# Kernel tuning notes

Measured on AMD Instinct MI355X. Metric: run time of the kernel, lower is better.

Reference implementation:

```python
import jax, jax.numpy as jnp
import numpy as np

D_MODEL = 1024
NUM_HEADS = 16
HEAD_DIM = D_MODEL // NUM_HEADS


def setup_inputs() -> dict:
    key = jax.random.key(0)
    ks = jax.random.split(key, 9)
    B, S, D = 2, 2048, D_MODEL
    s = 1.0 / np.sqrt(D)
    return {
        "x": jax.random.normal(ks[0], (B, S, D), dtype=jnp.float32),
        "Wq": jax.random.normal(ks[1], (D, D), dtype=jnp.float32) * s,
        "bq": jnp.zeros((D,), dtype=jnp.float32),
        "Wk": jax.random.normal(ks[2], (D, D), dtype=jnp.float32) * s,
        "bk": jnp.zeros((D,), dtype=jnp.float32),
        "Wv": jax.random.normal(ks[3], (D, D), dtype=jnp.float32) * s,
        "bv": jnp.zeros((D,), dtype=jnp.float32),
        "Wo": jax.random.normal(ks[4], (D, D), dtype=jnp.float32) * s,
        "bo": jnp.zeros((D,), dtype=jnp.float32),
    }


def reference(x, Wq, bq, Wk, bk, Wv, bv, Wo, bo):
    B, S, D = x.shape
    H, Hd = NUM_HEADS, HEAD_DIM
    # Linear projections (torch Linear: x @ W^T + b)
    q = (x @ Wq.T + bq).reshape(B, S, H, Hd).transpose(0, 2, 1, 3)  # [B,H,S,Hd]
    k = (x @ Wk.T + bk).reshape(B, S, H, Hd).transpose(0, 2, 1, 3)
    v = (x @ Wv.T + bv).reshape(B, S, H, Hd).transpose(0, 2, 1, 3)
    scale = 1.0 / jnp.sqrt(jnp.asarray(Hd, dtype=x.dtype))
    scores = jnp.einsum("bhqd,bhkd->bhqk", q, k) * scale  # [B,H,S,S]
    causal = jnp.triu(jnp.ones((S, S), dtype=bool), k=1)  # True above diagonal
    scores = jnp.where(causal[None, None], -jnp.inf, scores)
    attn = jax.nn.softmax(scores, axis=-1)
    out = jnp.einsum("bhqk,bhkd->bhqd", attn, v)  # [B,H,S,Hd]
    out = out.transpose(0, 2, 1, 3).reshape(B, S, D)
    return out @ Wo.T + bo
```

## Files before the change

kernel.cpp:

```cpp
#include <hip/hip_runtime.h>

typedef _Float16 f16x8 __attribute__((ext_vector_type(8)));
typedef _Float16 f16x4 __attribute__((ext_vector_type(4)));
typedef float f32x4 __attribute__((ext_vector_type(4)));

#define MFMA32(a, b, c) __builtin_amdgcn_mfma_f32_16x16x32_f16(a, b, c, 0, 0, 0)
#define MFMA16(a, b, c) __builtin_amdgcn_mfma_f32_16x16x16f16(a, b, c, 0, 0, 0)

__global__ __launch_bounds__(256) void convert_all(
    const float* __restrict__ x,
    const float* __restrict__ w0, const float* __restrict__ w1,
    const float* __restrict__ w2, const float* __restrict__ w3,
    _Float16* __restrict__ xb,
    _Float16* __restrict__ o0, _Float16* __restrict__ o1,
    _Float16* __restrict__ o2, _Float16* __restrict__ o3) {
  int chunk = blockIdx.x * 256 + threadIdx.x;
  const float* in;
  _Float16* out;
  int i;
  if (chunk < 1048576) {
    in = x; out = xb; i = chunk * 4;
  } else {
    int t = chunk - 1048576;
    int z = t >> 18;
    i = (t & 262143) * 4;
    in = (z == 0) ? w0 : (z == 1) ? w1 : (z == 2) ? w2 : w3;
    out = (z == 0) ? o0 : (z == 1) ? o1 : (z == 2) ? o2 : o3;
  }
  float4 v = *(const float4*)(in + i);
  f16x4 h;
  h.x = (_Float16)v.x; h.y = (_Float16)v.y; h.z = (_Float16)v.z; h.w = (_Float16)v.w;
  *(f16x4*)(out + i) = h;
}

__device__ __forceinline__ void gld_lds16(_Float16* l, const _Float16* g) {
  __builtin_amdgcn_global_load_lds(
      (const __attribute__((address_space(1))) unsigned int*)g,
      (__attribute__((address_space(3))) unsigned int*)l, 16, 0, 0);
}

__device__ __forceinline__ void stage64(_Float16* lds, const _Float16* g,
                                        int wid, int lane) {
#pragma unroll
  for (int j = 0; j < 2; ++j) {
    int blk = wid * 2 + j;
    int row = blk * 8 + (lane >> 3);
    int col = (lane & 7) * 8;
    gld_lds16(lds + blk * 512, g + (size_t)row * 1024 + col);
  }
}

__device__ __forceinline__ void stage128(_Float16* lds, const _Float16* g,
                                         int wid, int lane) {
#pragma unroll
  for (int j = 0; j < 4; ++j) {
    int blk = wid * 4 + j;
    int row = blk * 8 + (lane >> 3);
    int col = (lane & 7) * 8;
    gld_lds16(lds + blk * 512, g + (size_t)row * 1024 + col);
  }
}

__device__ __forceinline__ void gemm_core64(const _Float16* __restrict__ A,
                                            const _Float16* __restrict__ W,
                                            _Float16* As, _Float16* Bs,
                                            f32x4 acc[4][2], int m0, int n0, int tid) {
  int lane = tid & 63, wid = tid >> 6;
  int lr = lane & 15, lg = lane >> 4;
  int wn = wid * 32;
  for (int k0 = 0; k0 < 1024; k0 += 64) {
    __syncthreads();
    stage64(As, A + (size_t)m0 * 1024 + k0, wid, lane);
    stage128(Bs, W + (size_t)n0 * 1024 + k0, wid, lane);
    __syncthreads();
#pragma unroll
    for (int ks = 0; ks < 2; ++ks) {
      f16x8 af[4], bfv[2];
#pragma unroll
      for (int mf = 0; mf < 4; ++mf)
        af[mf] = *(const f16x8*)(As + (mf * 16 + lr) * 64 + ks * 32 + lg * 8);
#pragma unroll
      for (int nf = 0; nf < 2; ++nf)
        bfv[nf] = *(const f16x8*)(Bs + (wn + nf * 16 + lr) * 64 + ks * 32 + lg * 8);
#pragma unroll
      for (int mf = 0; mf < 4; ++mf)
#pragma unroll
        for (int nf = 0; nf < 2; ++nf)
          acc[mf][nf] = MFMA32(af[mf], bfv[nf], acc[mf][nf]);
    }
  }
}

#define TRP 72

__global__ __launch_bounds__(256) void proj_gemm(
    const _Float16* __restrict__ xb,
    const _Float16* __restrict__ wq, const _Float16* __restrict__ wk,
    const _Float16* __restrict__ wv,
    const float* __restrict__ bq, const float* __restrict__ bk,
    const float* __restrict__ bv,
    _Float16* __restrict__ qo, _Float16* __restrict__ ko, _Float16* __restrict__ vo) {
  __shared__ __align__(16) _Float16 smem[12288];
  _Float16* As = smem;
  _Float16* Bs = smem + 4096;
  int z = blockIdx.z;
  const _Float16* W = (z == 0) ? wq : ((z == 1) ? wk : wv);
  const float* bias = (z == 0) ? bq : ((z == 1) ? bk : bv);
  int tid = threadIdx.x;
  int m0 = blockIdx.x * 64, n0 = blockIdx.y * 128;
  f32x4 acc[4][2] = {};
  gemm_core64(xb, W, As, Bs, acc, m0, n0, tid);

  int lane = tid & 63, wid = tid >> 6;
  int lr = lane & 15, lg = lane >> 4;
  int wn = wid * 32;

  if (z == 2) {
    _Float16* Tr = smem;
    int b = m0 >> 11, s0 = m0 & 2047;
    __syncthreads();
#pragma unroll
    for (int nf = 0; nf < 2; ++nf) {
      int c = wn + nf * 16 + lr;
      float bb = bias[n0 + c];
#pragma unroll
      for (int mf = 0; mf < 4; ++mf)
#pragma unroll
        for (int i = 0; i < 4; ++i)
          Tr[c * TRP + mf * 16 + lg * 4 + i] = (_Float16)(acc[mf][nf][i] + bb);
    }
    __syncthreads();
#pragma unroll
    for (int j = 0; j < 4; ++j) {
      int cid = tid + 256 * j;
      int c = cid >> 3, seg = cid & 7;
      int cg = n0 + c, h = cg >> 6, hd = cg & 63;
      f16x8 v = *(const f16x8*)(Tr + c * TRP + seg * 8);
      *(f16x8*)(vo + ((size_t)(b * 16 + h) * 64 + hd) * 2048 + s0 + seg * 8) = v;
    }
  } else {
    _Float16* o = (z == 0) ? qo : ko;
#pragma unroll
    for (int nf = 0; nf < 2; ++nf) {
      int col = n0 + wn + nf * 16 + lr;
      float bb = bias[col];
      int h = col >> 6, hd = col & 63;
#pragma unroll
      for (int mf = 0; mf < 4; ++mf)
#pragma unroll
        for (int i = 0; i < 4; ++i) {
          int row = m0 + mf * 16 + lg * 4 + i;
          int b = row >> 11, s = row & 2047;
          o[((size_t)(b * 16 + h) * 2048 + s) * 64 + hd] = (_Float16)(acc[mf][nf][i] + bb);
        }
    }
  }
}

__global__ __launch_bounds__(256) void out_gemm(
    const _Float16* __restrict__ attn, const _Float16* __restrict__ wo,
    const float* __restrict__ bo, float* __restrict__ out) {
  __shared__ __align__(16) _Float16 smem[12288];
  _Float16* As = smem;
  _Float16* Bs = smem + 4096;
  int tid = threadIdx.x;
  int m0 = blockIdx.x * 64, n0 = blockIdx.y * 128;
  f32x4 acc[4][2] = {};
  gemm_core64(attn, wo, As, Bs, acc, m0, n0, tid);

  int lane = tid & 63, wid = tid >> 6;
  int lr = lane & 15, lg = lane >> 4;
  int wn = wid * 32;
#pragma unroll
  for (int nf = 0; nf < 2; ++nf) {
    int col = n0 + wn + nf * 16 + lr;
    float bb = bo[col];
#pragma unroll
    for (int mf = 0; mf < 4; ++mf)
#pragma unroll
      for (int i = 0; i < 4; ++i) {
        int row = m0 + mf * 16 + lg * 4 + i;
        out[(size_t)row * 1024 + col] = acc[mf][nf][i] + bb;
      }
  }
}

#define LDP 72

template <bool MASK>
__device__ __forceinline__ void attn_tile32(const _Float16* Ks, const _Float16* Vs,
                                            const f16x8 qb[2][2], int kv0, int qwb,
                                            int lr, int lg,
                                            float m[2], float l[2], f32x4 ot[2][4]) {
  const float L2E = 1.44269504f;
  const float NINF = -__builtin_inff();
  f16x8 kf0[4], kf1[4];
#pragma unroll
  for (int nf = 0; nf < 4; ++nf) {
    kf0[nf] = *(const f16x8*)(Ks + (nf * 16 + lr) * LDP + lg * 8);
    kf1[nf] = *(const f16x8*)(Ks + (nf * 16 + lr) * LDP + 32 + lg * 8);
  }
  f32x4 sc[2][4];
  __builtin_amdgcn_s_setprio(1);
#pragma unroll
  for (int h = 0; h < 2; ++h)
#pragma unroll
    for (int nf = 0; nf < 4; ++nf) {
      f32x4 z = {0.f, 0.f, 0.f, 0.f};
      z = MFMA32(kf0[nf], qb[h][0], z);
      z = MFMA32(kf1[nf], qb[h][1], z);
      sc[h][nf] = z;
    }
  __builtin_amdgcn_s_setprio(0);
  if (MASK) {
#pragma unroll
    for (int h = 0; h < 2; ++h) {
      int qg = qwb + h * 16 + lr;
#pragma unroll
      for (int nf = 0; nf < 4; ++nf)
#pragma unroll
        for (int i = 0; i < 4; ++i) {
          int kg = kv0 + nf * 16 + lg * 4 + i;
          sc[h][nf][i] = (kg <= qg) ? sc[h][nf][i] : NINF;
        }
    }
  }
  f16x4 pf[2][4];
#pragma unroll
  for (int h = 0; h < 2; ++h) {
    f32x4 mx4 = sc[h][0];
#pragma unroll
    for (int nf = 1; nf < 4; ++nf)
#pragma unroll
      for (int i = 0; i < 4; ++i) mx4[i] = fmaxf(mx4[i], sc[h][nf][i]);
    float tm = fmaxf(fmaxf(mx4[0], mx4[1]), fmaxf(mx4[2], mx4[3]));
    tm = fmaxf(tm, __shfl_xor(tm, 16));
    tm = fmaxf(tm, __shfl_xor(tm, 32));
    float mn = fmaxf(m[h], tm);
    float alpha = __builtin_amdgcn_exp2f((m[h] - mn) * L2E);
    m[h] = mn;
    float mnL = mn * L2E;
    float ps = 0.f;
#pragma unroll
    for (int nf = 0; nf < 4; ++nf)
#pragma unroll
      for (int i = 0; i < 4; ++i) {
        float p = __builtin_amdgcn_exp2f(sc[h][nf][i] * L2E - mnL);
        ps += p;
        pf[h][nf][i] = (_Float16)p;
      }
    ps += __shfl_xor(ps, 16);
    ps += __shfl_xor(ps, 32);
    l[h] = l[h] * alpha + ps;
#pragma unroll
    for (int dt = 0; dt < 4; ++dt)
#pragma unroll
      for (int i = 0; i < 4; ++i) ot[h][dt][i] *= alpha;
  }
  __builtin_amdgcn_s_setprio(1);
#pragma unroll
  for (int nf = 0; nf < 4; ++nf)
#pragma unroll
    for (int dt = 0; dt < 4; ++dt) {
      f16x4 vf = *(const f16x4*)(Vs + (dt * 16 + lr) * LDP + nf * 16 + lg * 4);
      ot[0][dt] = MFMA16(vf, pf[0][nf], ot[0][dt]);
      ot[1][dt] = MFMA16(vf, pf[1][nf], ot[1][dt]);
    }
  __builtin_amdgcn_s_setprio(0);
}

__global__ __launch_bounds__(256) void attn_kernel(
    const _Float16* __restrict__ Q, const _Float16* __restrict__ K,
    const _Float16* __restrict__ VT, _Float16* __restrict__ O) {
  __shared__ __align__(16) _Float16 Ks[2][64 * LDP];
  __shared__ __align__(16) _Float16 Vs[2][64 * LDP];
  int tid = threadIdx.x, lane = tid & 63, wid = tid >> 6;
  int qt = blockIdx.z ? (15 - (int)blockIdx.x) : (int)blockIdx.x;
  int hh = blockIdx.y, b = blockIdx.z;
  size_t hoff = (size_t)(b * 16 + hh) * 2048 * 64;
  const _Float16* Qh = Q + hoff;
  const _Float16* Kh = K + hoff;
  const _Float16* VTh = VT + hoff;
  int qwb = qt * 128 + wid * 32;
  int lr = lane & 15, lg = lane >> 4;

  f16x8 qb[2][2];
#pragma unroll
  for (int h = 0; h < 2; ++h) {
    const _Float16* qp = Qh + (size_t)(qwb + h * 16 + lr) * 64;
    qb[h][0] = *(const f16x8*)(qp + lg * 8);
    qb[h][1] = *(const f16x8*)(qp + 32 + lg * 8);
#pragma unroll
    for (int j = 0; j < 8; ++j) {
      qb[h][0][j] *= (_Float16)0.125f;
      qb[h][1][j] *= (_Float16)0.125f;
    }
  }

  float m[2] = {-__builtin_inff(), -__builtin_inff()};
  float l[2] = {0.f, 0.f};
  f32x4 ot[2][4] = {};

  int r0 = tid >> 3, c0 = (tid & 7) * 8;
  int r1 = r0 + 32;
  int4 rk0 = *(const int4*)(Kh + (size_t)r0 * 64 + c0);
  int4 rk1 = *(const int4*)(Kh + (size_t)r1 * 64 + c0);
  int4 rv0 = *(const int4*)(VTh + (size_t)r0 * 2048 + c0);
  int4 rv1 = *(const int4*)(VTh + (size_t)r1 * 2048 + c0);
  *(int4*)(&Ks[0][0] + r0 * LDP + c0) = rk0;
  *(int4*)(&Ks[0][0] + r1 * LDP + c0) = rk1;
  *(int4*)(&Vs[0][0] + r0 * LDP + c0) = rv0;
  *(int4*)(&Vs[0][0] + r1 * LDP + c0) = rv1;
  __syncthreads();

  int aw = qwb >> 6;
  int ntiles = 2 * qt + 2;
  for (int t = 0; t < ntiles; ++t) {
    int cur = t & 1;
    if (t + 1 < ntiles) {
      int nkv = (t + 1) * 64;
      rk0 = *(const int4*)(Kh + (size_t)(nkv + r0) * 64 + c0);
      rk1 = *(const int4*)(Kh + (size_t)(nkv + r1) * 64 + c0);
      rv0 = *(const int4*)(VTh + (size_t)r0 * 2048 + nkv + c0);
      rv1 = *(const int4*)(VTh + (size_t)r1 * 2048 + nkv + c0);
    }
    if (t < aw)
      attn_tile32<false>(&Ks[cur][0], &Vs[cur][0], qb, t * 64, qwb, lr, lg, m, l, ot);
    else if (t == aw)
      attn_tile32<true>(&Ks[cur][0], &Vs[cur][0], qb, t * 64, qwb, lr, lg, m, l, ot);
    if (t + 1 < ntiles) {
      *(int4*)(&Ks[cur ^ 1][0] + r0 * LDP + c0) = rk0;
      *(int4*)(&Ks[cur ^ 1][0] + r1 * LDP + c0) = rk1;
      *(int4*)(&Vs[cur ^ 1][0] + r0 * LDP + c0) = rv0;
      *(int4*)(&Vs[cur ^ 1][0] + r1 * LDP + c0) = rv1;
    }
    __syncthreads();
  }

#pragma unroll
  for (int h = 0; h < 2; ++h) {
    float inv = 1.f / l[h];
    _Float16* Oh = O + ((size_t)b * 2048 + qwb + h * 16 + lr) * 1024 + hh * 64;
#pragma unroll
    for (int dt = 0; dt < 4; ++dt) {
      f16x4 o;
#pragma unroll
      for (int i = 0; i < 4; ++i) o[i] = (_Float16)(ot[h][dt][i] * inv);
      *(f16x4*)(Oh + dt * 16 + lg * 4) = o;
    }
  }
}

extern "C" void kernel_launch(void* const* d_in, const int* in_sizes, int n_in,
                              void* d_out, int out_size, void* d_ws, size_t ws_size,
                              hipStream_t stream) {
  const float* x  = (const float*)d_in[0];
  const float* Wq = (const float*)d_in[1];
  const float* bq = (const float*)d_in[2];
  const float* Wk = (const float*)d_in[3];
  const float* bk = (const float*)d_in[4];
  const float* Wv = (const float*)d_in[5];
  const float* bv = (const float*)d_in[6];
  const float* Wo = (const float*)d_in[7];
  const float* bo = (const float*)d_in[8];
  float* out = (float*)d_out;

  _Float16* ws  = (_Float16*)d_ws;
  _Float16* xb  = ws;
  _Float16* wqb = ws + 4194304;
  _Float16* wkb = ws + 5242880;
  _Float16* wvb = ws + 6291456;
  _Float16* wob = ws + 7340032;
  _Float16* qw  = ws + 8388608;
  _Float16* kw  = ws + 12582912;
  _Float16* vtw = ws + 16777216;
  _Float16* aw  = ws + 20971520;

  convert_all<<<8192, 256, 0, stream>>>(x, Wq, Wk, Wv, Wo,
                                        xb, wqb, wkb, wvb, wob);

  proj_gemm<<<dim3(64, 8, 3), 256, 0, stream>>>(xb, wqb, wkb, wvb, bq, bk, bv,
                                                qw, kw, vtw);
  attn_kernel<<<dim3(16, 16, 2), 256, 0, stream>>>(qw, kw, vtw, aw);
  out_gemm<<<dim3(64, 8), 256, 0, stream>>>(aw, wob, bo, out);
}
```

Measured before the change: 127.6 us.

## Split causal attention KV range across two blocks and merge with combine kernel

Each query tile's causal KV range is split into two halves, each handled by its own block. The grid grows from 512 to 1024 blocks, and the causal work is balanced between the two halves. Each half writes unnormalized fp16 partial outputs plus per-row (max, sum) statistics into reused workspace buffers. A new combine kernel rescales and merges the two partials into the final attention output. The aim is more parallelism and better CU fill, at the cost of extra partial-output memory traffic, an extra launch, and fp16 storage of unnormalized accumulators.

```diff
diff --git a/kernel.cpp b/kernel.cpp
--- a/kernel.cpp
+++ b/kernel.cpp
@@ -271,12 +271,15 @@
 
 __global__ __launch_bounds__(256) void attn_kernel(
     const _Float16* __restrict__ Q, const _Float16* __restrict__ K,
-    const _Float16* __restrict__ VT, _Float16* __restrict__ O) {
+    const _Float16* __restrict__ VT,
+    _Float16* __restrict__ PO0, _Float16* __restrict__ PO1,
+    float2* __restrict__ ML) {
   __shared__ __align__(16) _Float16 Ks[2][64 * LDP];
   __shared__ __align__(16) _Float16 Vs[2][64 * LDP];
   int tid = threadIdx.x, lane = tid & 63, wid = tid >> 6;
-  int qt = blockIdx.z ? (15 - (int)blockIdx.x) : (int)blockIdx.x;
-  int hh = blockIdx.y, b = blockIdx.z;
+  int b = blockIdx.z >> 1, half = blockIdx.z & 1;
+  int qt = b ? (15 - (int)blockIdx.x) : (int)blockIdx.x;
+  int hh = blockIdx.y;
   size_t hoff = (size_t)(b * 16 + hh) * 2048 * 64;
   const _Float16* Qh = Q + hoff;
   const _Float16* Kh = K + hoff;
@@ -284,6 +287,9 @@
   int qwb = qt * 128 + wid * 32;
   int lr = lane & 15, lg = lane >> 4;
 
+  int start = half ? (qt + 1) : 0;
+  int end = half ? (2 * qt + 2) : (qt + 1);
+
   f16x8 qb[2][2];
 #pragma unroll
   for (int h = 0; h < 2; ++h) {
@@ -303,21 +309,24 @@
 
   int r0 = tid >> 3, c0 = (tid & 7) * 8;
   int r1 = r0 + 32;
-  int4 rk0 = *(const int4*)(Kh + (size_t)r0 * 64 + c0);
-  int4 rk1 = *(const int4*)(Kh + (size_t)r1 * 64 + c0);
-  int4 rv0 = *(const int4*)(VTh + (size_t)r0 * 2048 + c0);
-  int4 rv1 = *(const int4*)(VTh + (size_t)r1 * 2048 + c0);
-  *(int4*)(&Ks[0][0] + r0 * LDP + c0) = rk0;
-  *(int4*)(&Ks[0][0] + r1 * LDP + c0) = rk1;
-  *(int4*)(&Vs[0][0] + r0 * LDP + c0) = rv0;
-  *(int4*)(&Vs[0][0] + r1 * LDP + c0) = rv1;
+  {
+    int kv = start * 64;
+    int4 k0 = *(const int4*)(Kh + (size_t)(kv + r0) * 64 + c0);
+    int4 k1 = *(const int4*)(Kh + (size_t)(kv + r1) * 64 + c0);
+    int4 v0 = *(const int4*)(VTh + (size_t)r0 * 2048 + kv + c0);
+    int4 v1 = *(const int4*)(VTh + (size_t)r1 * 2048 + kv + c0);
+    *(int4*)(&Ks[0][0] + r0 * LDP + c0) = k0;
+    *(int4*)(&Ks[0][0] + r1 * LDP + c0) = k1;
+    *(int4*)(&Vs[0][0] + r0 * LDP + c0) = v0;
+    *(int4*)(&Vs[0][0] + r1 * LDP + c0) = v1;
+  }
   __syncthreads();
 
   int aw = qwb >> 6;
-  int ntiles = 2 * qt + 2;
-  for (int t = 0; t < ntiles; ++t) {
-    int cur = t & 1;
-    if (t + 1 < ntiles) {
+  int4 rk0, rk1, rv0, rv1;
+  for (int t = start; t < end; ++t) {
+    int cur = (t - start) & 1;
+    if (t + 1 < end) {
       int nkv = (t + 1) * 64;
       rk0 = *(const int4*)(Kh + (size_t)(nkv + r0) * 64 + c0);
       rk1 = *(const int4*)(Kh + (size_t)(nkv + r1) * 64 + c0);
@@ -328,7 +337,7 @@
       attn_tile32<false>(&Ks[cur][0], &Vs[cur][0], qb, t * 64, qwb, lr, lg, m, l, ot);
     else if (t == aw)
       attn_tile32<true>(&Ks[cur][0], &Vs[cur][0], qb, t * 64, qwb, lr, lg, m, l, ot);
-    if (t + 1 < ntiles) {
+    if (t + 1 < end) {
       *(int4*)(&Ks[cur ^ 1][0] + r0 * LDP + c0) = rk0;
       *(int4*)(&Ks[cur ^ 1][0] + r1 * LDP + c0) = rk1;
       *(int4*)(&Vs[cur ^ 1][0] + r0 * LDP + c0) = rv0;
@@ -337,18 +346,45 @@
     __syncthreads();
   }
 
+  _Float16* PO = half ? PO1 : PO0;
 #pragma unroll
   for (int h = 0; h < 2; ++h) {
-    float inv = 1.f / l[h];
-    _Float16* Oh = O + ((size_t)b * 2048 + qwb + h * 16 + lr) * 1024 + hh * 64;
+    int q = qwb + h * 16 + lr;
+    if (lg == 0)
+      ML[(((size_t)(half * 2 + b) * 2048 + q) << 4) + hh] = float2{m[h], l[h]};
+    _Float16* Oh = PO + ((size_t)b * 2048 + q) * 1024 + hh * 64;
 #pragma unroll
     for (int dt = 0; dt < 4; ++dt) {
       f16x4 o;
 #pragma unroll
-      for (int i = 0; i < 4; ++i) o[i] = (_Float16)(ot[h][dt][i] * inv);
+      for (int i = 0; i < 4; ++i) o[i] = (_Float16)ot[h][dt][i];
       *(f16x4*)(Oh + dt * 16 + lg * 4) = o;
     }
   }
+}
+
+__global__ __launch_bounds__(256) void attn_combine(
+    const _Float16* __restrict__ PO0, const _Float16* __restrict__ PO1,
+    const float2* __restrict__ ML, _Float16* __restrict__ Oout) {
+  const float L2E = 1.44269504f;
+  int g = blockIdx.x * 256 + threadIdx.x;
+  int row = g >> 3, chunk = g & 7;
+  float2 a = ML[row];
+  float2 c = ML[row + 65536];
+  float ms = fmaxf(a.x, c.x);
+  float f0 = __builtin_amdgcn_exp2f((a.x - ms) * L2E);
+  float f1 = __builtin_amdgcn_exp2f((c.x - ms) * L2E);
+  float inv = 1.f / (f0 * a.y + f1 * c.y);
+  f0 *= inv; f1 *= inv;
+  int b = row >> 15, q = (row >> 4) & 2047, h = row & 15;
+  size_t off = ((size_t)(b * 2048 + q) * 1024) + h * 64 + chunk * 8;
+  f16x8 o0 = *(const f16x8*)(PO0 + off);
+  f16x8 o1 = *(const f16x8*)(PO1 + off);
+  f16x8 r;
+#pragma unroll
+  for (int j = 0; j < 8; ++j)
+    r[j] = (_Float16)(f0 * (float)o0[j] + f1 * (float)o1[j]);
+  *(f16x8*)(Oout + off) = r;
 }
 
 extern "C" void kernel_launch(void* const* d_in, const int* in_sizes, int n_in,
@@ -376,11 +412,15 @@
   _Float16* vtw = ws + 16777216;
   _Float16* aw  = ws + 20971520;
 
+  _Float16* po0 = xb;
+  float2*   ml  = (float2*)wvb;
+
   convert_all<<<8192, 256, 0, stream>>>(x, Wq, Wk, Wv, Wo,
                                         xb, wqb, wkb, wvb, wob);
 
   proj_gemm<<<dim3(64, 8, 3), 256, 0, stream>>>(xb, wqb, wkb, wvb, bq, bk, bv,
                                                 qw, kw, vtw);
-  attn_kernel<<<dim3(16, 16, 2), 256, 0, stream>>>(qw, kw, vtw, aw);
+  attn_kernel<<<dim3(16, 16, 4), 256, 0, stream>>>(qw, kw, vtw, po0, aw, ml);
+  attn_combine<<<2048, 256, 0, stream>>>(po0, aw, ml, aw);
   out_gemm<<<dim3(64, 8), 256, 0, stream>>>(aw, wob, bo, out);
 }
```

After: 137.4 us, median of 2. 1.08x slower.
